# Optimization experiments

Measured on AMD Instinct MI355X. Metric: run time of the kernel, lower is better.

The kernel has to match this reference:

```python
import jax, jax.numpy as jnp
import numpy as np

N_NODES = 100000
N_EDGES = 1000000
IN_F = 64
OUT_F = 64
N_REL = 32
N_BASES = 30


def setup_inputs() -> dict:
    key = jax.random.key(0)
    k = jax.random.split(key, 8)
    node_features = jax.random.normal(k[0], (N_NODES, IN_F), dtype=jnp.float32)
    senders = jax.random.randint(k[1], (N_EDGES,), 0, N_NODES, dtype=jnp.int32)
    receivers = jax.random.randint(k[2], (N_EDGES,), 0, N_NODES, dtype=jnp.int32)
    relation_types = jax.random.randint(k[3], (N_EDGES,), 0, N_REL, dtype=jnp.int32)
    basis = jax.random.normal(k[4], (N_BASES, IN_F, OUT_F), dtype=jnp.float32) * 0.01
    coeff = jax.random.normal(k[5], (N_REL, N_BASES), dtype=jnp.float32) * 0.01
    self_weight = jax.random.normal(k[6], (IN_F, OUT_F), dtype=jnp.float32) * 0.01
    bias = jnp.zeros((OUT_F,), dtype=jnp.float32)
    return {
        "node_features": node_features,
        "senders": senders,
        "receivers": receivers,
        "relation_types": relation_types,
        "basis": basis,
        "coeff": coeff,
        "self_weight": self_weight,
        "bias": bias,
    }


def reference(node_features, senders, receivers, relation_types, basis, coeff, self_weight, bias):
    # R-GCN with basis decomposition: W_r = sum_b coeff[r,b] * basis[b].
    # The original loops over relations, masking edges; by linearity this equals
    # segment-summing source features per (receiver, relation) pair and then
    # contracting once with the relation weights -- same math, single pass.
    num_nodes = node_features.shape[0]
    n_edges = senders.shape[0]

    rel_weights = jnp.einsum('rb,bio->rio', coeff, basis)        # (R, in, out)
    src_features = node_features[senders]                         # (E, in)

    # segment id = receiver * R + relation -> (N*R, in) aggregate
    seg_ids = receivers * N_REL + relation_types
    agg = jax.ops.segment_sum(src_features, seg_ids, num_segments=num_nodes * N_REL)
    agg = agg.reshape(num_nodes, N_REL, node_features.shape[1])   # (N, R, in)

    aggregated = jnp.einsum('nri,rio->no', agg, rel_weights)      # (N, out)

    ones = jnp.ones((n_edges,), dtype=node_features.dtype)
    in_degree = jax.ops.segment_sum(ones, receivers, num_segments=num_nodes)
    in_degree = jnp.maximum(in_degree, 1.0)

    out = aggregated / in_degree[:, None]
    out = out + node_features @ self_weight
    out = out + bias
    return out
```

## Files before the change

kernel.cpp:

```cpp
#include <hip/hip_runtime.h>

#define N_F     64
#define N_REL   32
#define BLOCK   256
#define SCAN_TILE 2048

typedef __attribute__((ext_vector_type(8))) short bf16x8;
typedef __attribute__((ext_vector_type(4))) float f32x4;

__device__ __forceinline__ unsigned short f2bf(float f) {
    unsigned u = __float_as_uint(f);
    u += 0x7FFF + ((u >> 16) & 1);
    return (unsigned short)(u >> 16);
}

__global__ void __launch_bounds__(BLOCK) k_pre(const float* __restrict__ nf,
                                               const int* __restrict__ rel,
                                               const int* __restrict__ rcv,
                                               const float* __restrict__ basis,
                                               const float* __restrict__ coeff,
                                               unsigned short* __restrict__ xbf,
                                               unsigned short* __restrict__ Wsh,
                                               int* __restrict__ cnt1,
                                               int* __restrict__ cnt2,
                                               int E, int total4,
                                               int nbCast, int nbRelw) {
    const int bid = blockIdx.x;
    if (bid < nbCast) {
        int i = bid * BLOCK + threadIdx.x;
        if (i < total4) {
            float4 v = ((const float4*)nf)[i];
            ushort4 o;
            o.x = f2bf(v.x); o.y = f2bf(v.y); o.z = f2bf(v.z); o.w = f2bf(v.w);
            ((ushort4*)xbf)[i] = o;
        }
    } else if (bid < nbCast + nbRelw) {
        int idx = (bid - nbCast) * BLOCK + threadIdx.x;
        if (idx < N_REL * N_F * N_F) {
            int r  = idx >> 12;
            int io = idx & 4095;
            int k  = io >> 6;
            int n  = io & 63;
            float acc = 0.f;
#pragma unroll
            for (int b = 0; b < 30; ++b)
                acc += coeff[r * 30 + b] * basis[b * (N_F * N_F) + io];
            int ks = k >> 5, kk = k & 31;
            int nt = n >> 4, nl = n & 15;
            int lane = ((kk >> 3) << 4) | nl;
            int j    = kk & 7;
            Wsh[((((r * 2 + ks) * 4 + nt) * 64 + lane) << 3) + j] = f2bf(acc);
        }
    } else {
        __shared__ int h[N_REL];
        if (threadIdx.x < N_REL) h[threadIdx.x] = 0;
        __syncthreads();
        int e = (bid - nbCast - nbRelw) * BLOCK + threadIdx.x;
        if (e < E) {
            atomicAdd(&h[rel[e]], 1);
            atomicAdd(&cnt2[rcv[e]], 1);
        }
        __syncthreads();
        if (threadIdx.x < N_REL && h[threadIdx.x])
            atomicAdd(&cnt1[threadIdx.x], h[threadIdx.x]);
    }
}

__global__ void k_scan_sums(const int* __restrict__ cur, int* __restrict__ part,
                            int nbins) {
    __shared__ int red[BLOCK];
    int base = blockIdx.x * SCAN_TILE;
    int s = 0;
    for (int i = threadIdx.x; i < SCAN_TILE; i += BLOCK) {
        int idx = base + i;
        s += (idx < nbins) ? cur[idx] : 0;
    }
    red[threadIdx.x] = s;
    __syncthreads();
    for (int off = BLOCK / 2; off > 0; off >>= 1) {
        if (threadIdx.x < off) red[threadIdx.x] += red[threadIdx.x + off];
        __syncthreads();
    }
    if (threadIdx.x == 0) part[blockIdx.x] = red[0];
}

__global__ void k_scan_mid(const int* __restrict__ cnt1, int* __restrict__ base1,
                           int* __restrict__ cur1, int* __restrict__ part,
                           int* __restrict__ esrc, int* __restrict__ perm,
                           int npart, int Ppad) {
    __shared__ int buf[BLOCK];
    __shared__ int sbase[N_REL + 1];
    __shared__ int stotal;
    const int tid = threadIdx.x;

    int v = (tid < npart) ? part[tid] : 0;
    buf[tid] = v;
    __syncthreads();
    for (int off = 1; off < BLOCK; off <<= 1) {
        int t = (tid >= off) ? buf[tid - off] : 0;
        __syncthreads();
        buf[tid] += t;
        __syncthreads();
    }
    if (tid < npart) part[tid] = buf[tid] - v;

    if (tid == 0) {
        int acc = 0;
        for (int r = 0; r < N_REL; ++r) {
            base1[r] = acc;
            cur1[r]  = acc;
            sbase[r] = acc;
            acc += (cnt1[r] + 15) & ~15;
        }
        base1[N_REL] = Ppad;
        sbase[N_REL] = Ppad;
        stotal = acc;
    }
    __syncthreads();

    for (int i = tid; i < N_REL * 16; i += BLOCK) {
        int r = i >> 4, o = i & 15;
        int c  = cnt1[r];
        int p0 = sbase[r] + c;
        int p1 = sbase[r] + ((c + 15) & ~15);
        int p  = p0 + o;
        if (p < p1) { perm[p] = -1; esrc[p] = 0; }
    }
    for (int p = stotal + tid; p < Ppad; p += BLOCK) {
        perm[p] = -1; esrc[p] = 0;
    }
}

__global__ void k_scan_apply_tile(int* __restrict__ cur, const int* __restrict__ part,
                                  const int* __restrict__ base1,
                                  unsigned char* __restrict__ trel,
                                  int nbins, int npart, int T) {
    if ((int)blockIdx.x >= npart) {
        int t = (blockIdx.x - npart) * BLOCK + threadIdx.x;
        if (t < T) {
            int p = t << 4;
            int r = 0;
#pragma unroll
            for (int i = 1; i < N_REL; ++i) r += (p >= base1[i]);
            trel[t] = (unsigned char)r;
        }
        return;
    }
    __shared__ int buf[BLOCK];
    int base_t = blockIdx.x * SCAN_TILE + threadIdx.x * 8;
    int loc[8];
    int s = 0;
#pragma unroll
    for (int j = 0; j < 8; ++j) {
        int idx = base_t + j;
        int v = (idx < nbins) ? cur[idx] : 0;
        loc[j] = s;
        s += v;
    }
    buf[threadIdx.x] = s;
    __syncthreads();
    for (int off = 1; off < BLOCK; off <<= 1) {
        int t = (threadIdx.x >= off) ? buf[threadIdx.x - off] : 0;
        __syncthreads();
        buf[threadIdx.x] += t;
        __syncthreads();
    }
    int excl = buf[threadIdx.x] - s + part[blockIdx.x];
#pragma unroll
    for (int j = 0; j < 8; ++j) {
        int idx = base_t + j;
        if (idx < nbins) cur[idx] = loc[j] + excl;
    }
}

__global__ void k_scatter1(const int* __restrict__ snd, const int* __restrict__ rcv,
                           const int* __restrict__ rel, int* __restrict__ cur1,
                           int* __restrict__ cur2,
                           int* __restrict__ esrc, int* __restrict__ perm, int E) {
    __shared__ int h[N_REL], hb[N_REL];
    if (threadIdx.x < N_REL) h[threadIdx.x] = 0;
    __syncthreads();
    int e = blockIdx.x * blockDim.x + threadIdx.x;
    int r = -1;
    if (e < E) { r = rel[e]; atomicAdd(&h[r], 1); }
    __syncthreads();
    if (threadIdx.x < N_REL && h[threadIdx.x])
        hb[threadIdx.x] = atomicAdd(&cur1[threadIdx.x], h[threadIdx.x]);
    __syncthreads();
    if (threadIdx.x < N_REL) h[threadIdx.x] = 0;
    __syncthreads();
    if (e < E) {
        int rank = atomicAdd(&h[r], 1);
        int pos1 = hb[r] + rank;
        int pos2 = atomicAdd(&cur2[rcv[e]], 1);
        esrc[pos1] = snd[e];
        perm[pos1] = pos2;
    }
}

__global__ void __launch_bounds__(BLOCK) k_gemm(const unsigned short* __restrict__ xbf,
                                                const int* __restrict__ esrc,
                                                const int* __restrict__ perm,
                                                const unsigned char* __restrict__ trel,
                                                const unsigned short* __restrict__ Wsh,
                                                unsigned short* __restrict__ eoutb,
                                                int T, int tpw, int dumprow) {
    __shared__ float ts[4][16 * 68];
    const int tid  = threadIdx.x;
    const int lane = tid & 63;
    const int wave = tid >> 6;
    float* tb = ts[wave];

    const int gw = blockIdx.x * 4 + wave;
    const int t0 = gw * tpw;
    const int t1 = min(t0 + tpw, T);
    if (t0 >= T) return;

    const int row = lane & 15;
    const int kg  = lane >> 4;
    const int rr  = lane >> 2;
    const int ch  = lane & 3;

    int curR = -1;
    bf16x8 wf[2][4];

    int s_cur  = esrc[(t0 << 4) + row];
    int pm_cur = perm[(t0 << 4) + row];

    for (int t = t0; t < t1; ++t) {
        int s_nxt = 0, pm_nxt = -1;
        if (t + 1 < t1) {
            s_nxt  = esrc[((t + 1) << 4) + row];
            pm_nxt = perm[((t + 1) << 4) + row];
        }

        const int r = trel[t];
        if (r != curR) {
            curR = r;
#pragma unroll
            for (int ks = 0; ks < 2; ++ks)
#pragma unroll
                for (int nt = 0; nt < 4; ++nt)
                    wf[ks][nt] = *(const bf16x8*)(Wsh + ((((r * 2 + ks) * 4 + nt) * 64 + lane) << 3));
        }

        const size_t xb = ((size_t)s_cur << 6) + (kg << 3);
        bf16x8 a0 = *(const bf16x8*)(xbf + xb);
        bf16x8 a1 = *(const bf16x8*)(xbf + xb + 32);

        f32x4 acc[4];
#pragma unroll
        for (int nt = 0; nt < 4; ++nt) {
            acc[nt] = (f32x4){0.f, 0.f, 0.f, 0.f};
            acc[nt] = __builtin_amdgcn_mfma_f32_16x16x32_bf16(a0, wf[0][nt], acc[nt], 0, 0, 0);
            acc[nt] = __builtin_amdgcn_mfma_f32_16x16x32_bf16(a1, wf[1][nt], acc[nt], 0, 0, 0);
        }

#pragma unroll
        for (int nt = 0; nt < 4; ++nt)
#pragma unroll
            for (int reg = 0; reg < 4; ++reg)
                tb[(kg * 4 + reg) * 68 + nt * 16 + (lane & 15)] = acc[nt][reg];

        asm volatile("s_waitcnt lgkmcnt(0)" ::: "memory");

        int pmr = __shfl(pm_cur, rr);
        pmr = (pmr < 0) ? dumprow : pmr;

        const float* src = tb + rr * 68 + ch * 16;
        unsigned pk[8];
#pragma unroll
        for (int q = 0; q < 4; ++q) {
            float4 v = *(const float4*)(src + q * 4);
            pk[2 * q]     = (unsigned)f2bf(v.x) | ((unsigned)f2bf(v.y) << 16);
            pk[2 * q + 1] = (unsigned)f2bf(v.z) | ((unsigned)f2bf(v.w) << 16);
        }
        unsigned short* dst = eoutb + (size_t)pmr * 64 + ch * 16;
        uint4 v0; v0.x = pk[0]; v0.y = pk[1]; v0.z = pk[2]; v0.w = pk[3];
        uint4 v1; v1.x = pk[4]; v1.y = pk[5]; v1.z = pk[6]; v1.w = pk[7];
        *(uint4*)dst       = v0;
        *(uint4*)(dst + 8) = v1;

        s_cur = s_nxt; pm_cur = pm_nxt;
    }
}

__global__ void __launch_bounds__(BLOCK) k_recv(const unsigned short* __restrict__ xbf,
                                                const unsigned short* __restrict__ eoutb,
                                                const int* __restrict__ cur2,
                                                const float* __restrict__ selfw,
                                                const float* __restrict__ bias,
                                                float* __restrict__ out,
                                                int N, int rpw) {
    const int tid  = threadIdx.x;
    const int lane = tid & 63;
    const int wave = tid >> 6;
    const int gw   = blockIdx.x * 4 + wave;
    const int n0   = gw * rpw;
    const int n1   = min(n0 + rpw, N);
    if (n0 >= N) return;

    const int g = lane >> 5;
    const int c = lane & 31;

    float swcol[N_F];
#pragma unroll
    for (int i = 0; i < N_F; ++i) swcol[i] = selfw[i * N_F + lane];
    const float bv = bias[lane];

    int bidx = n0 - 1 + lane;
    int bnd  = 0;
    if (bidx >= 0 && bidx < N && lane <= (n1 - n0)) bnd = cur2[bidx];

    for (int n = n0; n < n1; ++n) {
        const int li = n - n0;
        const int st = __shfl(bnd, li);
        const int en = __shfl(bnd, li + 1);

        float a0 = 0.f, a1 = 0.f;
        int j = st;
        for (; j + 4 <= en; j += 4) {
            unsigned u0 = *(const unsigned*)(eoutb + ((size_t)(j + g)     << 6) + (c << 1));
            unsigned u1 = *(const unsigned*)(eoutb + ((size_t)(j + 2 + g) << 6) + (c << 1));
            a0 += __uint_as_float(u0 << 16) + __uint_as_float(u1 << 16);
            a1 += __uint_as_float(u0 & 0xFFFF0000u) + __uint_as_float(u1 & 0xFFFF0000u);
        }
        for (; j < en; j += 2) {
            int row = j + g;
            unsigned u = *(const unsigned*)(eoutb + ((size_t)row << 6) + (c << 1));
            if (row < en) {
                a0 += __uint_as_float(u << 16);
                a1 += __uint_as_float(u & 0xFFFF0000u);
            }
        }
        a0 += __shfl_xor(a0, 32);
        a1 += __shfl_xor(a1, 32);
        float v0 = __shfl(a0, lane >> 1);
        float v1 = __shfl(a1, lane >> 1);
        float agg = (lane & 1) ? v1 : v0;

        const uint4* xr = (const uint4*)(xbf + ((size_t)n << 6));
        float s0 = 0.f, s1 = 0.f, s2 = 0.f, s3 = 0.f;
#pragma unroll
        for (int q = 0; q < 8; ++q) {
            uint4 u = xr[q];
            float x0 = __uint_as_float(u.x << 16);
            float x1 = __uint_as_float(u.x & 0xFFFF0000u);
            float x2 = __uint_as_float(u.y << 16);
            float x3 = __uint_as_float(u.y & 0xFFFF0000u);
            float x4 = __uint_as_float(u.z << 16);
            float x5 = __uint_as_float(u.z & 0xFFFF0000u);
            float x6 = __uint_as_float(u.w << 16);
            float x7 = __uint_as_float(u.w & 0xFFFF0000u);
            s0 = __builtin_fmaf(x0, swcol[8 * q + 0], s0);
            s1 = __builtin_fmaf(x1, swcol[8 * q + 1], s1);
            s2 = __builtin_fmaf(x2, swcol[8 * q + 2], s2);
            s3 = __builtin_fmaf(x3, swcol[8 * q + 3], s3);
            s0 = __builtin_fmaf(x4, swcol[8 * q + 4], s0);
            s1 = __builtin_fmaf(x5, swcol[8 * q + 5], s1);
            s2 = __builtin_fmaf(x6, swcol[8 * q + 6], s2);
            s3 = __builtin_fmaf(x7, swcol[8 * q + 7], s3);
        }

        float dg  = (float)(en - st);
        float inv = 1.f / (dg < 1.f ? 1.f : dg);
        out[(size_t)n * N_F + lane] = agg * inv + (s0 + s1) + (s2 + s3) + bv;
    }
}

extern "C" void kernel_launch(void* const* d_in, const int* in_sizes, int n_in,
                              void* d_out, int out_size, void* d_ws, size_t ws_size,
                              hipStream_t stream) {
    const float* nf    = (const float*)d_in[0];
    const int*   snd   = (const int*)  d_in[1];
    const int*   rcv   = (const int*)  d_in[2];
    const int*   rel   = (const int*)  d_in[3];
    const float* basis = (const float*)d_in[4];
    const float* coeff = (const float*)d_in[5];
    const float* selfw = (const float*)d_in[6];
    const float* bias  = (const float*)d_in[7];
    float*       out   = (float*)d_out;

    const int N = in_sizes[0] / N_F;
    const int E = in_sizes[1];
    const int Ppad = (E + N_REL * 15 + 15) & ~15;
    const int T    = Ppad >> 4;
    const int NPART = (N + SCAN_TILE - 1) / SCAN_TILE;
    const int total4 = N * N_F / 4;

    unsigned short* eoutb = (unsigned short*)d_ws;
    unsigned short* Wsh   = eoutb + (size_t)Ppad * N_F;
    unsigned short* xbf   = Wsh + (size_t)N_REL * N_F * N_F;
    int* base1 = (int*)(xbf + (size_t)N * N_F);
    int* cur1  = base1 + 64;
    int* part  = cur1 + 32;
    int* cnt1  = part + 256;
    int* cnt2  = cnt1 + 32;
    int* esrc  = cnt2 + N;
    int* perm  = esrc + Ppad;
    unsigned char* trel = (unsigned char*)(perm + Ppad);

    hipMemsetAsync(cnt1, 0, (size_t)(32 + N) * sizeof(int), stream);

    const int NB_CAST = (total4 + BLOCK - 1) / BLOCK;
    const int NB_RELW = (N_REL * N_F * N_F + BLOCK - 1) / BLOCK;
    const int NB_HIST = (E + BLOCK - 1) / BLOCK;
    k_pre<<<NB_CAST + NB_RELW + NB_HIST, BLOCK, 0, stream>>>(
        nf, rel, rcv, basis, coeff, xbf, Wsh, cnt1, cnt2, E, total4, NB_CAST, NB_RELW);

    k_scan_sums<<<NPART, BLOCK, 0, stream>>>(cnt2, part, N);
    k_scan_mid <<<1,     BLOCK, 0, stream>>>(cnt1, base1, cur1, part, esrc, perm, NPART, Ppad);

    const int NB_TREL = (T + BLOCK - 1) / BLOCK;
    k_scan_apply_tile<<<NPART + NB_TREL, BLOCK, 0, stream>>>(cnt2, part, base1, trel, N, NPART, T);

    k_scatter1<<<(E + BLOCK - 1) / BLOCK, BLOCK, 0, stream>>>(snd, rcv, rel, cur1, cnt2,
                                                              esrc, perm, E);

    const int GEMM_BLOCKS = 1024;
    const int tpw = (T + GEMM_BLOCKS * 4 - 1) / (GEMM_BLOCKS * 4);
    k_gemm<<<GEMM_BLOCKS, BLOCK, 0, stream>>>(xbf, esrc, perm, trel, Wsh, eoutb, T, tpw, E);

    const int RECV_BLOCKS = 2048;
    const int rpw = (N + RECV_BLOCKS * 4 - 1) / (RECV_BLOCKS * 4);
    k_recv<<<RECV_BLOCKS, BLOCK, 0, stream>>>(xbf, eoutb, cnt2, selfw, bias, out, N, rpw);
}
```

Baseline: 372.2 us.

## Precompute per-block relation offsets via joint scan, remove global atomics in scatter

Each histogram block now writes its per-relation counts into an extended scan array placed after the receiver counts. A single prefix scan over both gives each scatter block a deterministic base offset per relation, so the scatter kernel no longer issues global atomicAdds on the 32 relation cursors and needs fewer barriers. The GEMM and receive kernels also get twice as many blocks. In exchange the scan covers more elements, about 125k extra, and the offset arithmetic depends on the receiver-count prefix summing to E.

Result: faster. 345.2 us (-7.3%).

```diff
diff --git a/kernel.cpp b/kernel.cpp
--- a/kernel.cpp
+++ b/kernel.cpp
@@ -22,8 +22,8 @@
                                                unsigned short* __restrict__ xbf,
                                                unsigned short* __restrict__ Wsh,
                                                int* __restrict__ cnt1,
-                                               int* __restrict__ cnt2,
-                                               int E, int total4,
+                                               int* __restrict__ S,
+                                               int E, int total4, int N, int nbh,
                                                int nbCast, int nbRelw) {
     const int bid = blockIdx.x;
     if (bid < nbCast) {
@@ -55,14 +55,18 @@
         __shared__ int h[N_REL];
         if (threadIdx.x < N_REL) h[threadIdx.x] = 0;
         __syncthreads();
-        int e = (bid - nbCast - nbRelw) * BLOCK + threadIdx.x;
+        const int bidh = bid - nbCast - nbRelw;
+        int e = bidh * BLOCK + threadIdx.x;
         if (e < E) {
             atomicAdd(&h[rel[e]], 1);
-            atomicAdd(&cnt2[rcv[e]], 1);
-        }
-        __syncthreads();
-        if (threadIdx.x < N_REL && h[threadIdx.x])
-            atomicAdd(&cnt1[threadIdx.x], h[threadIdx.x]);
+            atomicAdd(&S[rcv[e]], 1);
+        }
+        __syncthreads();
+        if (threadIdx.x < N_REL) {
+            int v = h[threadIdx.x];
+            S[N + threadIdx.x * nbh + bidh] = v;
+            if (v) atomicAdd(&cnt1[threadIdx.x], v);
+        }
     }
 }
 
@@ -85,7 +89,7 @@
 }
 
 __global__ void k_scan_mid(const int* __restrict__ cnt1, int* __restrict__ base1,
-                           int* __restrict__ cur1, int* __restrict__ part,
+                           int* __restrict__ ub1, int* __restrict__ part,
                            int* __restrict__ esrc, int* __restrict__ perm,
                            int npart, int Ppad) {
     __shared__ int buf[BLOCK];
@@ -105,15 +109,17 @@
     if (tid < npart) part[tid] = buf[tid] - v;
 
     if (tid == 0) {
-        int acc = 0;
+        int acc = 0, uacc = 0;
         for (int r = 0; r < N_REL; ++r) {
             base1[r] = acc;
-            cur1[r]  = acc;
             sbase[r] = acc;
-            acc += (cnt1[r] + 15) & ~15;
+            ub1[r]   = uacc;
+            acc  += (cnt1[r] + 15) & ~15;
+            uacc += cnt1[r];
         }
         base1[N_REL] = Ppad;
         sbase[N_REL] = Ppad;
+        ub1[N_REL]   = uacc;
         stotal = acc;
     }
     __syncthreads();
@@ -173,26 +179,29 @@
     }
 }
 
-__global__ void k_scatter1(const int* __restrict__ snd, const int* __restrict__ rcv,
-                           const int* __restrict__ rel, int* __restrict__ cur1,
-                           int* __restrict__ cur2,
-                           int* __restrict__ esrc, int* __restrict__ perm, int E) {
-    __shared__ int h[N_REL], hb[N_REL];
-    if (threadIdx.x < N_REL) h[threadIdx.x] = 0;
+__global__ void __launch_bounds__(BLOCK) k_scatter1(const int* __restrict__ snd,
+                                                    const int* __restrict__ rcv,
+                                                    const int* __restrict__ rel,
+                                                    int* S,
+                                                    const int* __restrict__ base1,
+                                                    const int* __restrict__ ub1,
+                                                    int* __restrict__ esrc,
+                                                    int* __restrict__ perm,
+                                                    int E, int N, int nbh) {
+    __shared__ int h[N_REL], bhb[N_REL];
+    const int b = blockIdx.x;
+    if (threadIdx.x < N_REL) {
+        int g = S[N + threadIdx.x * nbh + b];
+        bhb[threadIdx.x] = base1[threadIdx.x] + (g - E - ub1[threadIdx.x]);
+        h[threadIdx.x] = 0;
+    }
     __syncthreads();
-    int e = blockIdx.x * blockDim.x + threadIdx.x;
-    int r = -1;
-    if (e < E) { r = rel[e]; atomicAdd(&h[r], 1); }
-    __syncthreads();
-    if (threadIdx.x < N_REL && h[threadIdx.x])
-        hb[threadIdx.x] = atomicAdd(&cur1[threadIdx.x], h[threadIdx.x]);
-    __syncthreads();
-    if (threadIdx.x < N_REL) h[threadIdx.x] = 0;
-    __syncthreads();
+    int e = b * BLOCK + threadIdx.x;
     if (e < E) {
+        int r = rel[e];
         int rank = atomicAdd(&h[r], 1);
-        int pos1 = hb[r] + rank;
-        int pos2 = atomicAdd(&cur2[rcv[e]], 1);
+        int pos1 = bhb[r] + rank;
+        int pos2 = atomicAdd(&S[rcv[e]], 1);
         esrc[pos1] = snd[e];
         perm[pos1] = pos2;
     }
@@ -385,43 +394,48 @@
     const int E = in_sizes[1];
     const int Ppad = (E + N_REL * 15 + 15) & ~15;
     const int T    = Ppad >> 4;
-    const int NPART = (N + SCAN_TILE - 1) / SCAN_TILE;
     const int total4 = N * N_F / 4;
+
+    const int NB_CAST = (total4 + BLOCK - 1) / BLOCK;
+    const int NB_RELW = (N_REL * N_F * N_F + BLOCK - 1) / BLOCK;
+    const int NB_HIST = (E + BLOCK - 1) / BLOCK;
+    const int nbh     = NB_HIST;
+
+    const int SCAN_N = N + N_REL * nbh;
+    const int NPART  = (SCAN_N + SCAN_TILE - 1) / SCAN_TILE;
 
     unsigned short* eoutb = (unsigned short*)d_ws;
     unsigned short* Wsh   = eoutb + (size_t)Ppad * N_F;
     unsigned short* xbf   = Wsh + (size_t)N_REL * N_F * N_F;
     int* base1 = (int*)(xbf + (size_t)N * N_F);
-    int* cur1  = base1 + 64;
-    int* part  = cur1 + 32;
+    int* ub1   = base1 + 64;
+    int* part  = ub1 + 64;
     int* cnt1  = part + 256;
-    int* cnt2  = cnt1 + 32;
-    int* esrc  = cnt2 + N;
+    int* S     = cnt1 + 32;
+    int* esrc  = S + SCAN_N;
     int* perm  = esrc + Ppad;
     unsigned char* trel = (unsigned char*)(perm + Ppad);
 
-    hipMemsetAsync(cnt1, 0, (size_t)(32 + N) * sizeof(int), stream);
-
-    const int NB_CAST = (total4 + BLOCK - 1) / BLOCK;
-    const int NB_RELW = (N_REL * N_F * N_F + BLOCK - 1) / BLOCK;
-    const int NB_HIST = (E + BLOCK - 1) / BLOCK;
+    hipMemsetAsync(cnt1, 0, (size_t)(32 + SCAN_N) * sizeof(int), stream);
+
     k_pre<<<NB_CAST + NB_RELW + NB_HIST, BLOCK, 0, stream>>>(
-        nf, rel, rcv, basis, coeff, xbf, Wsh, cnt1, cnt2, E, total4, NB_CAST, NB_RELW);
-
-    k_scan_sums<<<NPART, BLOCK, 0, stream>>>(cnt2, part, N);
-    k_scan_mid <<<1,     BLOCK, 0, stream>>>(cnt1, base1, cur1, part, esrc, perm, NPART, Ppad);
+        nf, rel, rcv, basis, coeff, xbf, Wsh, cnt1, S, E, total4, N, nbh, NB_CAST, NB_RELW);
+
+    k_scan_sums<<<NPART, BLOCK, 0, stream>>>(S, part, SCAN_N);
+    k_scan_mid <<<1,     BLOCK, 0, stream>>>(cnt1, base1, ub1, part, esrc, perm, NPART, Ppad);
 
     const int NB_TREL = (T + BLOCK - 1) / BLOCK;
-    k_scan_apply_tile<<<NPART + NB_TREL, BLOCK, 0, stream>>>(cnt2, part, base1, trel, N, NPART, T);
-
-    k_scatter1<<<(E + BLOCK - 1) / BLOCK, BLOCK, 0, stream>>>(snd, rcv, rel, cur1, cnt2,
-                                                              esrc, perm, E);
-
-    const int GEMM_BLOCKS = 1024;
+    k_scan_apply_tile<<<NPART + NB_TREL, BLOCK, 0, stream>>>(S, part, base1, trel,
+                                                             SCAN_N, NPART, T);
+
+    k_scatter1<<<nbh, BLOCK, 0, stream>>>(snd, rcv, rel, S, base1, ub1, esrc, perm,
+                                          E, N, nbh);
+
+    const int GEMM_BLOCKS = 2048;
     const int tpw = (T + GEMM_BLOCKS * 4 - 1) / (GEMM_BLOCKS * 4);
     k_gemm<<<GEMM_BLOCKS, BLOCK, 0, stream>>>(xbf, esrc, perm, trel, Wsh, eoutb, T, tpw, E);
 
-    const int RECV_BLOCKS = 2048;
+    const int RECV_BLOCKS = 4096;
     const int rpw = (N + RECV_BLOCKS * 4 - 1) / (RECV_BLOCKS * 4);
-    k_recv<<<RECV_BLOCKS, BLOCK, 0, stream>>>(xbf, eoutb, cnt2, selfw, bias, out, N, rpw);
-}
+    k_recv<<<RECV_BLOCKS, BLOCK, 0, stream>>>(xbf, eoutb, S, selfw, bias, out, N, rpw);
+}
```
